# Performance work log

Measured on AMD Instinct MI355X. Metric: run time of the kernel, lower is better.

The kernel has to match this reference:

```python
import jax, jax.numpy as jnp
import numpy as np

SEQ, D_MODEL, N_HEADS, D_INT = 2048, 1024, 16, 64
D_OUT = D_MODEL // N_HEADS  # 64


def setup_inputs() -> dict:
    key = jax.random.key(0)
    ks = jax.random.split(key, 9)
    s = lambda fan_in: 1.0 / np.sqrt(fan_in)
    return {
        "input_vecs": jax.random.normal(ks[0], (8, SEQ, D_MODEL), dtype=jnp.float32),
        # weights stored [in, out] (torch Linear weight transposed)
        "Wk": jax.random.uniform(ks[1], (D_MODEL, D_INT), minval=-s(D_MODEL), maxval=s(D_MODEL)),
        "bk": jax.random.uniform(ks[2], (D_INT,), minval=-s(D_MODEL), maxval=s(D_MODEL)),
        "Wq": jax.random.uniform(ks[3], (D_MODEL, D_INT), minval=-s(D_MODEL), maxval=s(D_MODEL)),
        "bq": jax.random.uniform(ks[4], (D_INT,), minval=-s(D_MODEL), maxval=s(D_MODEL)),
        "Wv": jax.random.uniform(ks[5], (D_MODEL, D_INT), minval=-s(D_MODEL), maxval=s(D_MODEL)),
        "bv": jax.random.uniform(ks[6], (D_INT,), minval=-s(D_MODEL), maxval=s(D_MODEL)),
        "W0": jax.random.uniform(ks[7], (D_INT, D_OUT), minval=-s(D_INT), maxval=s(D_INT)),
        "b0": jax.random.uniform(ks[8], (D_OUT,), minval=-s(D_INT), maxval=s(D_INT)),
    }


def reference(input_vecs, Wk, bk, Wq, bq, Wv, bv, W0, b0):
    # Projections: [B, T, d_int]
    k = jnp.einsum("btd,de->bte", input_vecs, Wk) + bk
    q = jnp.einsum("btd,de->bte", input_vecs, Wq) + bq
    v = jnp.einsum("btd,de->bte", input_vecs, Wv) + bv
    d_k = k.shape[-1]
    # Causal scores: [B, T, T]
    scores = jnp.einsum("bqe,bke->bqk", q, k) * (d_k ** -0.5)
    T = scores.shape[-1]
    causal = jnp.tril(jnp.ones((T, T), dtype=bool))
    scores = jnp.where(causal, scores, -jnp.inf)
    attn = jax.nn.softmax(scores, axis=-1)
    ctx = jnp.einsum("bqk,bke->bqe", attn, v)  # [B, T, d_int]
    return jnp.einsum("bte,eo->bto", ctx, W0) + b0  # [B, T, d_model//num_heads]
```

## Files before the change

kernel.cpp:

```cpp
#include <hip/hip_runtime.h>
#include <math.h>

#define SEQ 2048
#define DM  1024
#define DI  64

typedef __attribute__((ext_vector_type(8))) short short8;
typedef __attribute__((ext_vector_type(4))) float f32x4;
typedef __attribute__((ext_vector_type(4))) unsigned short ush4;

#define MFMA16(a,b,c) __builtin_amdgcn_mfma_f32_16x16x32_bf16(a,b,c,0,0,0)

__device__ __forceinline__ unsigned short f2bf(float f) {
    unsigned int u = __builtin_bit_cast(unsigned int, f);
    u += 0x7fffu + ((u >> 16) & 1u);
    return (unsigned short)(u >> 16);
}


__global__ __launch_bounds__(256)
void convert_kernel(const float* __restrict__ Wq, const float* __restrict__ Wk,
                    const float* __restrict__ Wv, const float* __restrict__ W0,
                    const float* __restrict__ bq, const float* __restrict__ bk,
                    const float* __restrict__ bv,
                    unsigned short* __restrict__ Wf, unsigned short* __restrict__ W0f,
                    float* __restrict__ bcat)
{
    const int t = threadIdx.x;
    const int blk = blockIdx.x;
    if (blk < 96) {
        const int flat = blk * 256 + t;
        const int lane = flat & 63;
        const int s    = (flat >> 6) & 1;
        const int gk   = flat >> 7;
        const int g = gk >> 4, ks = gk & 15;
        const int n = lane & 15, quad = lane >> 4;
        const int ocat = 16 * g + n;
        const int mat = ocat >> 6, o = ocat & 63;
        const float* src = (mat == 0) ? Wq : (mat == 1) ? Wk : Wv;
        const float scale = (mat == 0) ? 0.125f : 1.0f;
        const int kb = ks * 64 + s * 32 + quad * 8;
        union { short8 v; unsigned short u[8]; } pk;
#pragma unroll
        for (int e = 0; e < 8; ++e)
            pk.u[e] = f2bf(src[(size_t)(kb + e) * DI + o] * scale);
        *(short8*)(Wf + (size_t)flat * 8) = pk.v;
    } else {
        const int flat = (blk - 96) * 256 + t;
        if (flat < 512) {
            const int lane = flat & 63;
            const int s    = (flat >> 6) & 1;
            const int g    = flat >> 7;
            const int n = lane & 15, quad = lane >> 4;
            const int o = 16 * g + n;
            const int kb = s * 32 + quad * 8;
            union { short8 v; unsigned short u[8]; } pk;
#pragma unroll
            for (int e = 0; e < 8; ++e)
                pk.u[e] = f2bf(W0[(size_t)(kb + e) * DI + o]);
            *(short8*)(W0f + (size_t)flat * 8) = pk.v;
        }
        if (blk == 96 && t < 192)
            bcat[t] = (t < 64) ? bq[t] * 0.125f : (t < 128) ? bk[t - 64] : bv[t - 128];
    }
}

__global__ __launch_bounds__(256, 2)
void proj_kernel(const float* __restrict__ X, const unsigned short* __restrict__ Wf,
                 const float* __restrict__ bcat,
                 unsigned short* __restrict__ Qf, unsigned short* __restrict__ Kf,
                 unsigned short* __restrict__ Vf)
{
    __shared__ alignas(16) unsigned char smem[32 * 200 * 2];
    unsigned short* XbS = (unsigned short*)smem;

    const int t = threadIdx.x;
    const int lane = t & 63, w = t >> 6;
    const int quad = lane >> 4, n = lane & 15;
    const int r0 = blockIdx.x * 32;

    const f32x4 ZERO = {0.f, 0.f, 0.f, 0.f};
    f32x4 acc[2][3];
#pragma unroll
    for (int a = 0; a < 2; ++a)
#pragma unroll
        for (int j = 0; j < 3; ++j) acc[a][j] = ZERO;

    const int srow = t >> 3, sg = t & 7;
    const int sslot = srow * 8 + (sg ^ (srow & 7));
    const float* xp = X + (size_t)(r0 + srow) * DM + sg * 8;

    for (int ks = 0; ks < 16; ++ks) {
        const int k0 = ks * 64;
        const float4 xa = *(const float4*)(xp + k0);
        const float4 xb = *(const float4*)(xp + k0 + 4);
        short8 bfr[3][2];
#pragma unroll
        for (int j = 0; j < 3; ++j)
#pragma unroll
            for (int s = 0; s < 2; ++s)
                bfr[j][s] = *(const short8*)(Wf + (size_t)((((3*w + j)*16 + ks)*2 + s)*64 + lane) * 8);
        __syncthreads();
        union { short8 v; unsigned short u[8]; } px;
        px.u[0] = f2bf(xa.x); px.u[1] = f2bf(xa.y); px.u[2] = f2bf(xa.z); px.u[3] = f2bf(xa.w);
        px.u[4] = f2bf(xb.x); px.u[5] = f2bf(xb.y); px.u[6] = f2bf(xb.z); px.u[7] = f2bf(xb.w);
        *(short8*)(XbS + sslot * 8) = px.v;
        __syncthreads();
        short8 af[2][2];
#pragma unroll
        for (int tt = 0; tt < 2; ++tt)
#pragma unroll
            for (int s = 0; s < 2; ++s) {
                const int slot = (tt*16 + n) * 8 + ((s*4 + quad) ^ (n & 7));
                af[tt][s] = *(const short8*)(XbS + slot * 8);
            }
#pragma unroll
        for (int tt = 0; tt < 2; ++tt)
#pragma unroll
            for (int j = 0; j < 3; ++j) {
                acc[tt][j] = MFMA16(af[tt][0], bfr[j][0], acc[tt][j]);
                acc[tt][j] = MFMA16(af[tt][1], bfr[j][1], acc[tt][j]);
            }
    }

    __syncthreads();
    unsigned short (*Facc)[200] = (unsigned short (*)[200])smem;
    float bias[3];
#pragma unroll
    for (int j = 0; j < 3; ++j) bias[j] = bcat[(3*w + j)*16 + n];
#pragma unroll
    for (int tt = 0; tt < 2; ++tt)
#pragma unroll
        for (int j = 0; j < 3; ++j)
#pragma unroll
            for (int r = 0; r < 4; ++r)
                Facc[tt*16 + quad*4 + r][(3*w + j)*16 + n] = f2bf(acc[tt][j][r] + bias[j]);
    __syncthreads();

    const int bidx = r0 >> 11;
    const int qt16 = (r0 >> 4) & 127;
    const int kc   = (r0 >> 6) & 31;
    const int sblk = (r0 >> 5) & 1;
    {
        const int qsel = t >> 7, s = (t >> 6) & 1, lp = t & 63;
        const int np = lp & 15, qp = lp >> 4;
        const int row = qsel * 16 + np, col = s * 32 + qp * 8;
        const size_t off = (size_t)(((bidx * 128 + qt16 + qsel) * 2 + s) * 64 + lp) * 8;
        *(short8*)(Qf + off) = *(const short8*)&Facc[row][col];
        *(short8*)(Kf + off) = *(const short8*)&Facc[row][64 + col];
    }
    {
        const int nt = t >> 6, lp = t & 63;
        const int np = lp & 15, qp = lp >> 4;
        union { short8 v; unsigned short u[8]; } ov;
#pragma unroll
        for (int e = 0; e < 8; ++e) ov.u[e] = Facc[qp * 8 + e][128 + 16 * nt + np];
        const size_t off = (size_t)((((bidx * 4 + nt) * 32 + kc) * 2 + sblk) * 64 + lp) * 8;
        *(short8*)(Vf + off) = ov.v;
    }
}

__global__ __launch_bounds__(256, 3)
void attn_kernel(const unsigned short* __restrict__ Qf, const unsigned short* __restrict__ Kf,
                 const unsigned short* __restrict__ Vf, const unsigned short* __restrict__ W0f,
                 const float* __restrict__ b0, float* __restrict__ Out)
{
    __shared__ alignas(16) float pool[4][32][72];
    __shared__ alignas(16) unsigned short Cb[32][72];
    __shared__ float Lp[4][32][4];

    const int t = threadIdx.x;
    const int lane = t & 63, w = t >> 6;
    const int quad = lane >> 4, n = lane & 15;
    const int qt = 63 - (blockIdx.x >> 3);
    const int b  = blockIdx.x & 7;
    const int q0 = qt * 32;

    unsigned short* P = (unsigned short*)&pool[w][0][0];

    short8 qf[2][2];
#pragma unroll
    for (int qh = 0; qh < 2; ++qh)
#pragma unroll
        for (int s = 0; s < 2; ++s)
            qf[qh][s] = *(const short8*)(Qf + (size_t)(((b*128 + qt*2 + qh)*2 + s)*64 + lane) * 8);

    const f32x4 ZERO = {0.f, 0.f, 0.f, 0.f};
    f32x4 ctx[2][4];
#pragma unroll
    for (int qh = 0; qh < 2; ++qh)
#pragma unroll
        for (int nt = 0; nt < 4; ++nt) ctx[qh][nt] = ZERO;
    float rs[2] = {0.f, 0.f};
    const float M0 = 8.0f;

    const int C = (qt >> 1) + 1;
    for (int kt = w; kt < C; kt += 4) {
        const int k0 = kt * 64;
        short8 kf[4][2];
#pragma unroll
        for (int tt = 0; tt < 4; ++tt)
#pragma unroll
            for (int s = 0; s < 2; ++s)
                kf[tt][s] = *(const short8*)(Kf + (size_t)(((b*128 + kt*4 + tt)*2 + s)*64 + lane) * 8);
        f32x4 sv[2][4];
#pragma unroll
        for (int qh = 0; qh < 2; ++qh)
#pragma unroll
            for (int tt = 0; tt < 4; ++tt) {
                f32x4 a = MFMA16(kf[tt][0], qf[qh][0], ZERO);
                sv[qh][tt] = MFMA16(kf[tt][1], qf[qh][1], a);
            }
        short8 vf[4][2];
#pragma unroll
        for (int nt = 0; nt < 4; ++nt)
#pragma unroll
            for (int s = 0; s < 2; ++s)
                vf[nt][s] = *(const short8*)(Vf + (size_t)((((b*4 + nt)*32 + kt)*2 + s)*64 + lane) * 8);
        if (kt == C - 1) {
#pragma unroll
            for (int qh = 0; qh < 2; ++qh)
#pragma unroll
                for (int tt = 0; tt < 4; ++tt)
#pragma unroll
                    for (int r = 0; r < 4; ++r)
                        if (k0 + 16*tt + quad*4 + r > q0 + qh*16 + n)
                            sv[qh][tt][r] = -INFINITY;
        }
#pragma unroll
        for (int qh = 0; qh < 2; ++qh)
#pragma unroll
            for (int tt = 0; tt < 4; ++tt) {
                union { ush4 v; unsigned short u[4]; } pw;
#pragma unroll
                for (int r = 0; r < 4; ++r) {
                    const float p = __expf(sv[qh][tt][r] - M0);
                    rs[qh] += p;
                    pw.u[r] = f2bf(p);
                }
                *(ush4*)&P[(size_t)(qh*16 + n) * 72 + 16*tt + quad*4] = pw.v;
            }
#pragma unroll
        for (int s = 0; s < 2; ++s) {
            const short8 pf0 = *(const short8*)&P[(size_t)(n)      * 72 + s*32 + quad*8];
            const short8 pf1 = *(const short8*)&P[(size_t)(16 + n) * 72 + s*32 + quad*8];
#pragma unroll
            for (int nt = 0; nt < 4; ++nt) {
                ctx[0][nt] = MFMA16(pf0, vf[nt][s], ctx[0][nt]);
                ctx[1][nt] = MFMA16(pf1, vf[nt][s], ctx[1][nt]);
            }
        }
    }
#pragma unroll
    for (int qh = 0; qh < 2; ++qh) {
#pragma unroll
        for (int nt = 0; nt < 4; ++nt)
#pragma unroll
            for (int r = 0; r < 4; ++r)
                pool[w][qh*16 + quad*4 + r][nt*16 + n] = ctx[qh][nt][r];
        Lp[w][qh*16 + n][quad] = rs[qh];
    }
    __syncthreads();

    {
        const int q = t >> 3, c0 = (t & 7) * 8;
        float l = 0.f;
#pragma unroll
        for (int w4 = 0; w4 < 4; ++w4)
#pragma unroll
            for (int qd = 0; qd < 4; ++qd) l += Lp[w4][q][qd];
        const float inv = 1.0f / l;
        float s[8];
#pragma unroll
        for (int j = 0; j < 8; ++j) s[j] = 0.f;
#pragma unroll
        for (int w4 = 0; w4 < 4; ++w4) {
            const float4 a = *(const float4*)&pool[w4][q][c0];
            const float4 c = *(const float4*)&pool[w4][q][c0 + 4];
            s[0] += a.x; s[1] += a.y; s[2] += a.z; s[3] += a.w;
            s[4] += c.x; s[5] += c.y; s[6] += c.z; s[7] += c.w;
        }
        union { short8 v; unsigned short u[8]; } cb;
#pragma unroll
        for (int j = 0; j < 8; ++j) cb.u[j] = f2bf(s[j] * inv);
        *(short8*)&Cb[q][c0] = cb.v;
    }
    __syncthreads();

    f32x4 oacc[2] = {ZERO, ZERO};
#pragma unroll
    for (int s = 0; s < 2; ++s) {
        const short8 wf = *(const short8*)(W0f + (size_t)((w*2 + s)*64 + lane) * 8);
#pragma unroll
        for (int tt = 0; tt < 2; ++tt) {
            const short8 cf = *(const short8*)&Cb[tt*16 + n][s*32 + quad*8];
            oacc[tt] = MFMA16(cf, wf, oacc[tt]);
        }
    }
    const float bb = b0[16*w + n];
#pragma unroll
    for (int tt = 0; tt < 2; ++tt)
#pragma unroll
        for (int r = 0; r < 4; ++r)
            Out[((size_t)b * SEQ + q0 + tt*16 + quad*4 + r) * DI + 16*w + n] = oacc[tt][r] + bb;
}

extern "C" void kernel_launch(void* const* d_in, const int* in_sizes, int n_in,
                              void* d_out, int out_size, void* d_ws, size_t ws_size,
                              hipStream_t stream) {
    const float* X  = (const float*)d_in[0];
    const float* Wk = (const float*)d_in[1];
    const float* bk = (const float*)d_in[2];
    const float* Wq = (const float*)d_in[3];
    const float* bq = (const float*)d_in[4];
    const float* Wv = (const float*)d_in[5];
    const float* bv = (const float*)d_in[6];
    const float* W0 = (const float*)d_in[7];
    const float* b0 = (const float*)d_in[8];
    float* Out = (float*)d_out;

    unsigned char* ws = (unsigned char*)d_ws;
    unsigned short* Wf   = (unsigned short*)ws;
    unsigned short* W0f  = (unsigned short*)(ws + 393216);
    float*          bcat = (float*)(ws + 401408);
    unsigned short* Qf   = (unsigned short*)(ws + 409600);
    unsigned short* Kf   = (unsigned short*)(ws + 409600 + 2097152);
    unsigned short* Vf   = (unsigned short*)(ws + 409600 + 4194304);

    convert_kernel<<<98, 256, 0, stream>>>(Wq, Wk, Wv, W0, bq, bk, bv, Wf, W0f, bcat);
    proj_kernel<<<512, 256, 0, stream>>>(X, Wf, bcat, Qf, Kf, Vf);
    attn_kernel<<<512, 256, 0, stream>>>(Qf, Kf, Vf, W0f, b0, Out);
}
```

Baseline: 134.2 us.

## Halve row tiles, double-buffer X and prefetch weights/K in proj and attention

Both the projection and attention kernels now work on 16-row tiles instead of 32 and launch twice as many blocks, with launch bounds raised to four blocks per CU. The projection kernel double-buffers the bf16 X tile in shared memory and prefetches the next weight fragments and the X rows two steps ahead, which removes one barrier per k-step. The attention kernel prefetches the next K tile in registers before computing the current one. The aim is better latency hiding and occupancy. The cost is that each MFMA fragment of K/V and weights is reused over fewer query rows, so global and L2 traffic per output rises.

```diff
diff --git a/kernel.cpp b/kernel.cpp
--- a/kernel.cpp
+++ b/kernel.cpp
@@ -65,244 +65,235 @@
     }
 }
 
-__global__ __launch_bounds__(256, 2)
+__global__ __launch_bounds__(256, 4)
 void proj_kernel(const float* __restrict__ X, const unsigned short* __restrict__ Wf,
                  const float* __restrict__ bcat,
                  unsigned short* __restrict__ Qf, unsigned short* __restrict__ Kf,
                  unsigned short* __restrict__ Vf)
 {
-    __shared__ alignas(16) unsigned char smem[32 * 200 * 2];
-    unsigned short* XbS = (unsigned short*)smem;
-
+    __shared__ alignas(16) unsigned short Xb[2][1024];
+    __shared__ alignas(16) unsigned short Facc[16][200];
     const int t = threadIdx.x;
     const int lane = t & 63, w = t >> 6;
     const int quad = lane >> 4, n = lane & 15;
-    const int r0 = blockIdx.x * 32;
+    const int r0 = blockIdx.x * 16;
+
+    const int tok = t >> 4, g = t & 15;
+    const int wslot = tok * 64 + (((g >> 1) ^ (tok & 7)) << 3) + (g & 1) * 4;
+    const float* xp = X + (size_t)(r0 + tok) * DM + g * 4;
+    const unsigned short* wbase = Wf + (size_t)(3 * w) * 16 * 1024 + lane * 8;
 
     const f32x4 ZERO = {0.f, 0.f, 0.f, 0.f};
-    f32x4 acc[2][3];
-#pragma unroll
-    for (int a = 0; a < 2; ++a)
-#pragma unroll
-        for (int j = 0; j < 3; ++j) acc[a][j] = ZERO;
-
-    const int srow = t >> 3, sg = t & 7;
-    const int sslot = srow * 8 + (sg ^ (srow & 7));
-    const float* xp = X + (size_t)(r0 + srow) * DM + sg * 8;
-
+    f32x4 acc[3] = {ZERO, ZERO, ZERO};
+
+    float4 x0 = *(const float4*)(xp);
+    float4 xA = *(const float4*)(xp + 64);
+    short8 wcur[3][2], wnxt[3][2];
+#pragma unroll
+    for (int j = 0; j < 3; ++j)
+#pragma unroll
+        for (int s = 0; s < 2; ++s)
+            wcur[j][s] = *(const short8*)(wbase + (size_t)((j * 16) * 2 + s) * 512);
+    {
+        union { ush4 v; unsigned short u[4]; } px;
+        px.u[0] = f2bf(x0.x); px.u[1] = f2bf(x0.y); px.u[2] = f2bf(x0.z); px.u[3] = f2bf(x0.w);
+        *(ush4*)&Xb[0][wslot] = px.v;
+    }
+    __syncthreads();
+
+#pragma unroll 2
     for (int ks = 0; ks < 16; ++ks) {
-        const int k0 = ks * 64;
-        const float4 xa = *(const float4*)(xp + k0);
-        const float4 xb = *(const float4*)(xp + k0 + 4);
-        short8 bfr[3][2];
+        const int kx = (ks + 2 < 16) ? ks + 2 : 15;
+        float4 xB = *(const float4*)(xp + kx * 64);
+        const int ksn = (ks + 1 < 16) ? ks + 1 : 15;
 #pragma unroll
         for (int j = 0; j < 3; ++j)
 #pragma unroll
             for (int s = 0; s < 2; ++s)
-                bfr[j][s] = *(const short8*)(Wf + (size_t)((((3*w + j)*16 + ks)*2 + s)*64 + lane) * 8);
+                wnxt[j][s] = *(const short8*)(wbase + (size_t)((j * 16 + ksn) * 2 + s) * 512);
+        short8 af[2];
+#pragma unroll
+        for (int s = 0; s < 2; ++s)
+            af[s] = *(const short8*)&Xb[ks & 1][n * 64 + (((s * 4 + quad) ^ (n & 7)) << 3)];
+#pragma unroll
+        for (int j = 0; j < 3; ++j) {
+            acc[j] = MFMA16(af[0], wcur[j][0], acc[j]);
+            acc[j] = MFMA16(af[1], wcur[j][1], acc[j]);
+        }
+        {
+            union { ush4 v; unsigned short u[4]; } px;
+            px.u[0] = f2bf(xA.x); px.u[1] = f2bf(xA.y); px.u[2] = f2bf(xA.z); px.u[3] = f2bf(xA.w);
+            *(ush4*)&Xb[(ks + 1) & 1][wslot] = px.v;
+        }
         __syncthreads();
-        union { short8 v; unsigned short u[8]; } px;
-        px.u[0] = f2bf(xa.x); px.u[1] = f2bf(xa.y); px.u[2] = f2bf(xa.z); px.u[3] = f2bf(xa.w);
-        px.u[4] = f2bf(xb.x); px.u[5] = f2bf(xb.y); px.u[6] = f2bf(xb.z); px.u[7] = f2bf(xb.w);
-        *(short8*)(XbS + sslot * 8) = px.v;
-        __syncthreads();
-        short8 af[2][2];
-#pragma unroll
-        for (int tt = 0; tt < 2; ++tt)
-#pragma unroll
-            for (int s = 0; s < 2; ++s) {
-                const int slot = (tt*16 + n) * 8 + ((s*4 + quad) ^ (n & 7));
-                af[tt][s] = *(const short8*)(XbS + slot * 8);
-            }
-#pragma unroll
-        for (int tt = 0; tt < 2; ++tt)
-#pragma unroll
-            for (int j = 0; j < 3; ++j) {
-                acc[tt][j] = MFMA16(af[tt][0], bfr[j][0], acc[tt][j]);
-                acc[tt][j] = MFMA16(af[tt][1], bfr[j][1], acc[tt][j]);
-            }
-    }
-
-    __syncthreads();
-    unsigned short (*Facc)[200] = (unsigned short (*)[200])smem;
-    float bias[3];
-#pragma unroll
-    for (int j = 0; j < 3; ++j) bias[j] = bcat[(3*w + j)*16 + n];
-#pragma unroll
-    for (int tt = 0; tt < 2; ++tt)
+        xA = xB;
 #pragma unroll
         for (int j = 0; j < 3; ++j)
 #pragma unroll
-            for (int r = 0; r < 4; ++r)
-                Facc[tt*16 + quad*4 + r][(3*w + j)*16 + n] = f2bf(acc[tt][j][r] + bias[j]);
+            for (int s = 0; s < 2; ++s) wcur[j][s] = wnxt[j][s];
+    }
+
+#pragma unroll
+    for (int j = 0; j < 3; ++j) {
+        const float bias = bcat[(3 * w + j) * 16 + n];
+#pragma unroll
+        for (int r = 0; r < 4; ++r)
+            Facc[quad * 4 + r][(3 * w + j) * 16 + n] = f2bf(acc[j][r] + bias);
+    }
     __syncthreads();
 
     const int bidx = r0 >> 11;
     const int qt16 = (r0 >> 4) & 127;
     const int kc   = (r0 >> 6) & 31;
     const int sblk = (r0 >> 5) & 1;
-    {
-        const int qsel = t >> 7, s = (t >> 6) & 1, lp = t & 63;
+    if (t < 128) {
+        const int s = t >> 6, lp = t & 63;
         const int np = lp & 15, qp = lp >> 4;
-        const int row = qsel * 16 + np, col = s * 32 + qp * 8;
-        const size_t off = (size_t)(((bidx * 128 + qt16 + qsel) * 2 + s) * 64 + lp) * 8;
-        *(short8*)(Qf + off) = *(const short8*)&Facc[row][col];
-        *(short8*)(Kf + off) = *(const short8*)&Facc[row][64 + col];
-    }
-    {
-        const int nt = t >> 6, lp = t & 63;
-        const int np = lp & 15, qp = lp >> 4;
+        const size_t off = (size_t)(((bidx * 128 + qt16) * 2 + s) * 64 + lp) * 8;
+        *(short8*)(Qf + off) = *(const short8*)&Facc[np][s * 32 + qp * 8];
+        *(short8*)(Kf + off) = *(const short8*)&Facc[np][64 + s * 32 + qp * 8];
+    } else {
+        const int i = t - 128;
+        const int nt = i >> 5, lp = i & 31;
+        const int q2 = (r0 & 31) >> 3;
+        const int quadp = q2 + (lp >> 4), np = lp & 15;
+        const int lanep = quadp * 16 + np;
         union { short8 v; unsigned short u[8]; } ov;
 #pragma unroll
-        for (int e = 0; e < 8; ++e) ov.u[e] = Facc[qp * 8 + e][128 + 16 * nt + np];
-        const size_t off = (size_t)((((bidx * 4 + nt) * 32 + kc) * 2 + sblk) * 64 + lp) * 8;
+        for (int e = 0; e < 8; ++e) ov.u[e] = Facc[(lp >> 4) * 8 + e][128 + 16 * nt + np];
+        const size_t off = (size_t)((((bidx * 4 + nt) * 32 + kc) * 2 + sblk) * 64 + lanep) * 8;
         *(short8*)(Vf + off) = ov.v;
     }
 }
 
-__global__ __launch_bounds__(256, 3)
+__global__ __launch_bounds__(256, 4)
 void attn_kernel(const unsigned short* __restrict__ Qf, const unsigned short* __restrict__ Kf,
                  const unsigned short* __restrict__ Vf, const unsigned short* __restrict__ W0f,
                  const float* __restrict__ b0, float* __restrict__ Out)
 {
-    __shared__ alignas(16) float pool[4][32][72];
-    __shared__ alignas(16) unsigned short Cb[32][72];
-    __shared__ float Lp[4][32][4];
+    __shared__ alignas(16) float pool[4][16][72];
+    __shared__ float Lp[4][16][4];
+    __shared__ alignas(16) unsigned short Cb[16][72];
 
     const int t = threadIdx.x;
     const int lane = t & 63, w = t >> 6;
     const int quad = lane >> 4, n = lane & 15;
-    const int qt = 63 - (blockIdx.x >> 3);
+    const int qt = 127 - (blockIdx.x >> 3);
     const int b  = blockIdx.x & 7;
-    const int q0 = qt * 32;
+    const int q0 = qt * 16;
 
     unsigned short* P = (unsigned short*)&pool[w][0][0];
 
-    short8 qf[2][2];
-#pragma unroll
-    for (int qh = 0; qh < 2; ++qh)
-#pragma unroll
-        for (int s = 0; s < 2; ++s)
-            qf[qh][s] = *(const short8*)(Qf + (size_t)(((b*128 + qt*2 + qh)*2 + s)*64 + lane) * 8);
+    short8 qf[2];
+#pragma unroll
+    for (int s = 0; s < 2; ++s)
+        qf[s] = *(const short8*)(Qf + (size_t)(((b * 128 + qt) * 2 + s) * 64 + lane) * 8);
 
     const f32x4 ZERO = {0.f, 0.f, 0.f, 0.f};
-    f32x4 ctx[2][4];
-#pragma unroll
-    for (int qh = 0; qh < 2; ++qh)
-#pragma unroll
-        for (int nt = 0; nt < 4; ++nt) ctx[qh][nt] = ZERO;
-    float rs[2] = {0.f, 0.f};
+    f32x4 ctx[4] = {ZERO, ZERO, ZERO, ZERO};
+    float rs = 0.f;
     const float M0 = 8.0f;
 
-    const int C = (qt >> 1) + 1;
+    const int C = (qt >> 2) + 1;
+    short8 kfc[4][2], kfn[4][2];
+    if (w < C) {
+#pragma unroll
+        for (int tt = 0; tt < 4; ++tt)
+#pragma unroll
+            for (int s = 0; s < 2; ++s)
+                kfc[tt][s] = *(const short8*)(Kf + (size_t)(((b * 128 + w * 4 + tt) * 2 + s) * 64 + lane) * 8);
+    }
     for (int kt = w; kt < C; kt += 4) {
+        const int ktn = (kt + 4 < C) ? kt + 4 : kt;
+#pragma unroll
+        for (int tt = 0; tt < 4; ++tt)
+#pragma unroll
+            for (int s = 0; s < 2; ++s)
+                kfn[tt][s] = *(const short8*)(Kf + (size_t)(((b * 128 + ktn * 4 + tt) * 2 + s) * 64 + lane) * 8);
+        short8 vf[4][2];
+#pragma unroll
+        for (int nt = 0; nt < 4; ++nt)
+#pragma unroll
+            for (int s = 0; s < 2; ++s)
+                vf[nt][s] = *(const short8*)(Vf + (size_t)((((b * 4 + nt) * 32 + kt) * 2 + s) * 64 + lane) * 8);
+
         const int k0 = kt * 64;
-        short8 kf[4][2];
+        f32x4 sv[4];
+#pragma unroll
+        for (int tt = 0; tt < 4; ++tt) {
+            f32x4 a = MFMA16(kfc[tt][0], qf[0], ZERO);
+            sv[tt] = MFMA16(kfc[tt][1], qf[1], a);
+        }
+        if (kt == C - 1) {
+#pragma unroll
+            for (int tt = 0; tt < 4; ++tt)
+#pragma unroll
+                for (int r = 0; r < 4; ++r)
+                    if (k0 + 16 * tt + quad * 4 + r > q0 + n) sv[tt][r] = -INFINITY;
+        }
+#pragma unroll
+        for (int tt = 0; tt < 4; ++tt) {
+            union { ush4 v; unsigned short u[4]; } pw;
+#pragma unroll
+            for (int r = 0; r < 4; ++r) {
+                const float p = __expf(sv[tt][r] - M0);
+                rs += p;
+                pw.u[r] = f2bf(p);
+            }
+            *(ush4*)&P[(size_t)n * 72 + 16 * tt + quad * 4] = pw.v;
+        }
+#pragma unroll
+        for (int s = 0; s < 2; ++s) {
+            const short8 pf = *(const short8*)&P[(size_t)n * 72 + s * 32 + quad * 8];
+#pragma unroll
+            for (int nt = 0; nt < 4; ++nt)
+                ctx[nt] = MFMA16(pf, vf[nt][s], ctx[nt]);
+        }
 #pragma unroll
         for (int tt = 0; tt < 4; ++tt)
 #pragma unroll
-            for (int s = 0; s < 2; ++s)
-                kf[tt][s] = *(const short8*)(Kf + (size_t)(((b*128 + kt*4 + tt)*2 + s)*64 + lane) * 8);
-        f32x4 sv[2][4];
-#pragma unroll
-        for (int qh = 0; qh < 2; ++qh)
-#pragma unroll
-            for (int tt = 0; tt < 4; ++tt) {
-                f32x4 a = MFMA16(kf[tt][0], qf[qh][0], ZERO);
-                sv[qh][tt] = MFMA16(kf[tt][1], qf[qh][1], a);
-            }
-        short8 vf[4][2];
-#pragma unroll
-        for (int nt = 0; nt < 4; ++nt)
-#pragma unroll
-            for (int s = 0; s < 2; ++s)
-                vf[nt][s] = *(const short8*)(Vf + (size_t)((((b*4 + nt)*32 + kt)*2 + s)*64 + lane) * 8);
-        if (kt == C - 1) {
-#pragma unroll
-            for (int qh = 0; qh < 2; ++qh)
-#pragma unroll
-                for (int tt = 0; tt < 4; ++tt)
-#pragma unroll
-                    for (int r = 0; r < 4; ++r)
-                        if (k0 + 16*tt + quad*4 + r > q0 + qh*16 + n)
-                            sv[qh][tt][r] = -INFINITY;
-        }
-#pragma unroll
-        for (int qh = 0; qh < 2; ++qh)
-#pragma unroll
-            for (int tt = 0; tt < 4; ++tt) {
-                union { ush4 v; unsigned short u[4]; } pw;
-#pragma unroll
-                for (int r = 0; r < 4; ++r) {
-                    const float p = __expf(sv[qh][tt][r] - M0);
-                    rs[qh] += p;
-                    pw.u[r] = f2bf(p);
-                }
-                *(ush4*)&P[(size_t)(qh*16 + n) * 72 + 16*tt + quad*4] = pw.v;
-            }
-#pragma unroll
-        for (int s = 0; s < 2; ++s) {
-            const short8 pf0 = *(const short8*)&P[(size_t)(n)      * 72 + s*32 + quad*8];
-            const short8 pf1 = *(const short8*)&P[(size_t)(16 + n) * 72 + s*32 + quad*8];
-#pragma unroll
-            for (int nt = 0; nt < 4; ++nt) {
-                ctx[0][nt] = MFMA16(pf0, vf[nt][s], ctx[0][nt]);
-                ctx[1][nt] = MFMA16(pf1, vf[nt][s], ctx[1][nt]);
-            }
-        }
-    }
-#pragma unroll
-    for (int qh = 0; qh < 2; ++qh) {
-#pragma unroll
-        for (int nt = 0; nt < 4; ++nt)
-#pragma unroll
-            for (int r = 0; r < 4; ++r)
-                pool[w][qh*16 + quad*4 + r][nt*16 + n] = ctx[qh][nt][r];
-        Lp[w][qh*16 + n][quad] = rs[qh];
-    }
+            for (int s = 0; s < 2; ++s) kfc[tt][s] = kfn[tt][s];
+    }
+#pragma unroll
+    for (int nt = 0; nt < 4; ++nt)
+#pragma unroll
+        for (int r = 0; r < 4; ++r)
+            pool[w][quad * 4 + r][nt * 16 + n] = ctx[nt][r];
+    Lp[w][n][quad] = rs;
     __syncthreads();
 
     {
-        const int q = t >> 3, c0 = (t & 7) * 8;
+        const int q = t >> 4, c0 = (t & 15) * 4;
         float l = 0.f;
 #pragma unroll
         for (int w4 = 0; w4 < 4; ++w4)
 #pragma unroll
             for (int qd = 0; qd < 4; ++qd) l += Lp[w4][q][qd];
         const float inv = 1.0f / l;
-        float s[8];
-#pragma unroll
-        for (int j = 0; j < 8; ++j) s[j] = 0.f;
+        float s[4] = {0.f, 0.f, 0.f, 0.f};
 #pragma unroll
         for (int w4 = 0; w4 < 4; ++w4) {
             const float4 a = *(const float4*)&pool[w4][q][c0];
-            const float4 c = *(const float4*)&pool[w4][q][c0 + 4];
             s[0] += a.x; s[1] += a.y; s[2] += a.z; s[3] += a.w;
-            s[4] += c.x; s[5] += c.y; s[6] += c.z; s[7] += c.w;
-        }
-        union { short8 v; unsigned short u[8]; } cb;
-#pragma unroll
-        for (int j = 0; j < 8; ++j) cb.u[j] = f2bf(s[j] * inv);
-        *(short8*)&Cb[q][c0] = cb.v;
+        }
+        union { ush4 v; unsigned short u[4]; } cb;
+#pragma unroll
+        for (int j = 0; j < 4; ++j) cb.u[j] = f2bf(s[j] * inv);
+        *(ush4*)&Cb[q][c0] = cb.v;
     }
     __syncthreads();
 
-    f32x4 oacc[2] = {ZERO, ZERO};
+    f32x4 oacc = ZERO;
 #pragma unroll
     for (int s = 0; s < 2; ++s) {
-        const short8 wf = *(const short8*)(W0f + (size_t)((w*2 + s)*64 + lane) * 8);
-#pragma unroll
-        for (int tt = 0; tt < 2; ++tt) {
-            const short8 cf = *(const short8*)&Cb[tt*16 + n][s*32 + quad*8];
-            oacc[tt] = MFMA16(cf, wf, oacc[tt]);
-        }
-    }
-    const float bb = b0[16*w + n];
-#pragma unroll
-    for (int tt = 0; tt < 2; ++tt)
-#pragma unroll
-        for (int r = 0; r < 4; ++r)
-            Out[((size_t)b * SEQ + q0 + tt*16 + quad*4 + r) * DI + 16*w + n] = oacc[tt][r] + bb;
+        const short8 cf = *(const short8*)&Cb[n][s * 32 + quad * 8];
+        const short8 wf = *(const short8*)(W0f + (size_t)((w * 2 + s) * 64 + lane) * 8);
+        oacc = MFMA16(cf, wf, oacc);
+    }
+    const float bb = b0[16 * w + n];
+#pragma unroll
+    for (int r = 0; r < 4; ++r)
+        Out[((size_t)b * SEQ + q0 + quad * 4 + r) * DI + 16 * w + n] = oacc[r] + bb;
 }
 
 extern "C" void kernel_launch(void* const* d_in, const int* in_sizes, int n_in,
@@ -328,6 +319,6 @@
     unsigned short* Vf   = (unsigned short*)(ws + 409600 + 4194304);
 
     convert_kernel<<<98, 256, 0, stream>>>(Wq, Wk, Wv, W0, bq, bk, bv, Wf, W0f, bcat);
-    proj_kernel<<<512, 256, 0, stream>>>(X, Wf, bcat, Qf, Kf, Vf);
-    attn_kernel<<<512, 256, 0, stream>>>(Qf, Kf, Vf, W0f, b0, Out);
-}
+    proj_kernel<<<1024, 256, 0, stream>>>(X, Wf, bcat, Qf, Kf, Vf);
+    attn_kernel<<<1024, 256, 0, stream>>>(Qf, Kf, Vf, W0f, b0, Out);
+}
```

Measured after the change: 144.3 us. 7.5% more time.

## Load X fragments directly into registers with software-pipelined prefetch in projection

Applied to the files above, without the earlier changes.

The projection kernel no longer stages X through shared memory with two barriers per k-step. Each wave loads its own X fragments from global memory straight into MFMA operand layout and converts them to bf16 in registers. X is prefetched two steps ahead and weights one step ahead to hide global latency. This raises register pressure, and each of the four waves now reads and converts the full X tile redundantly, which means four times the global X loads per block.

```diff
diff --git a/kernel.cpp b/kernel.cpp
--- a/kernel.cpp
+++ b/kernel.cpp
@@ -71,70 +71,99 @@
                  unsigned short* __restrict__ Qf, unsigned short* __restrict__ Kf,
                  unsigned short* __restrict__ Vf)
 {
-    __shared__ alignas(16) unsigned char smem[32 * 200 * 2];
-    unsigned short* XbS = (unsigned short*)smem;
-
+    __shared__ alignas(16) unsigned short Facc[32][200];
     const int t = threadIdx.x;
     const int lane = t & 63, w = t >> 6;
     const int quad = lane >> 4, n = lane & 15;
     const int r0 = blockIdx.x * 32;
 
+    const float* xr[2];
+    xr[0] = X + (size_t)(r0 + n) * DM + quad * 8;
+    xr[1] = X + (size_t)(r0 + 16 + n) * DM + quad * 8;
+    const unsigned short* wbase = Wf + (size_t)(3 * w) * 16 * 1024 + lane * 8;
+
     const f32x4 ZERO = {0.f, 0.f, 0.f, 0.f};
     f32x4 acc[2][3];
 #pragma unroll
-    for (int a = 0; a < 2; ++a)
-#pragma unroll
-        for (int j = 0; j < 3; ++j) acc[a][j] = ZERO;
-
-    const int srow = t >> 3, sg = t & 7;
-    const int sslot = srow * 8 + (sg ^ (srow & 7));
-    const float* xp = X + (size_t)(r0 + srow) * DM + sg * 8;
+    for (int th = 0; th < 2; ++th)
+#pragma unroll
+        for (int j = 0; j < 3; ++j) acc[th][j] = ZERO;
+
+    float4 xA[2][2][2], xB[2][2][2];
+    short8 wcur[3][2], wnxt[3][2];
+#pragma unroll
+    for (int th = 0; th < 2; ++th)
+#pragma unroll
+        for (int s = 0; s < 2; ++s) {
+            xA[th][s][0] = *(const float4*)(xr[th] + s * 32);
+            xA[th][s][1] = *(const float4*)(xr[th] + s * 32 + 4);
+            xB[th][s][0] = *(const float4*)(xr[th] + 64 + s * 32);
+            xB[th][s][1] = *(const float4*)(xr[th] + 64 + s * 32 + 4);
+        }
+#pragma unroll
+    for (int j = 0; j < 3; ++j)
+#pragma unroll
+        for (int s = 0; s < 2; ++s)
+            wcur[j][s] = *(const short8*)(wbase + (size_t)((j * 16) * 2 + s) * 512);
 
     for (int ks = 0; ks < 16; ++ks) {
-        const int k0 = ks * 64;
-        const float4 xa = *(const float4*)(xp + k0);
-        const float4 xb = *(const float4*)(xp + k0 + 4);
-        short8 bfr[3][2];
+        const int ksn = (ks + 1 < 16) ? ks + 1 : 15;
+        const int kx  = (ks + 2 < 16) ? ks + 2 : 15;
 #pragma unroll
         for (int j = 0; j < 3; ++j)
 #pragma unroll
             for (int s = 0; s < 2; ++s)
-                bfr[j][s] = *(const short8*)(Wf + (size_t)((((3*w + j)*16 + ks)*2 + s)*64 + lane) * 8);
-        __syncthreads();
-        union { short8 v; unsigned short u[8]; } px;
-        px.u[0] = f2bf(xa.x); px.u[1] = f2bf(xa.y); px.u[2] = f2bf(xa.z); px.u[3] = f2bf(xa.w);
-        px.u[4] = f2bf(xb.x); px.u[5] = f2bf(xb.y); px.u[6] = f2bf(xb.z); px.u[7] = f2bf(xb.w);
-        *(short8*)(XbS + sslot * 8) = px.v;
-        __syncthreads();
+                wnxt[j][s] = *(const short8*)(wbase + (size_t)((j * 16 + ksn) * 2 + s) * 512);
+        float4 xC[2][2][2];
+#pragma unroll
+        for (int th = 0; th < 2; ++th)
+#pragma unroll
+            for (int s = 0; s < 2; ++s) {
+                xC[th][s][0] = *(const float4*)(xr[th] + kx * 64 + s * 32);
+                xC[th][s][1] = *(const float4*)(xr[th] + kx * 64 + s * 32 + 4);
+            }
         short8 af[2][2];
 #pragma unroll
-        for (int tt = 0; tt < 2; ++tt)
+        for (int th = 0; th < 2; ++th)
 #pragma unroll
             for (int s = 0; s < 2; ++s) {
-                const int slot = (tt*16 + n) * 8 + ((s*4 + quad) ^ (n & 7));
-                af[tt][s] = *(const short8*)(XbS + slot * 8);
-            }
-#pragma unroll
-        for (int tt = 0; tt < 2; ++tt)
+                union { short8 v; unsigned short u[8]; } px;
+                px.u[0] = f2bf(xA[th][s][0].x); px.u[1] = f2bf(xA[th][s][0].y);
+                px.u[2] = f2bf(xA[th][s][0].z); px.u[3] = f2bf(xA[th][s][0].w);
+                px.u[4] = f2bf(xA[th][s][1].x); px.u[5] = f2bf(xA[th][s][1].y);
+                px.u[6] = f2bf(xA[th][s][1].z); px.u[7] = f2bf(xA[th][s][1].w);
+                af[th][s] = px.v;
+            }
+#pragma unroll
+        for (int th = 0; th < 2; ++th)
 #pragma unroll
             for (int j = 0; j < 3; ++j) {
-                acc[tt][j] = MFMA16(af[tt][0], bfr[j][0], acc[tt][j]);
-                acc[tt][j] = MFMA16(af[tt][1], bfr[j][1], acc[tt][j]);
-            }
-    }
-
-    __syncthreads();
-    unsigned short (*Facc)[200] = (unsigned short (*)[200])smem;
+                acc[th][j] = MFMA16(af[th][0], wcur[j][0], acc[th][j]);
+                acc[th][j] = MFMA16(af[th][1], wcur[j][1], acc[th][j]);
+            }
+#pragma unroll
+        for (int th = 0; th < 2; ++th)
+#pragma unroll
+            for (int s = 0; s < 2; ++s) {
+                xA[th][s][0] = xB[th][s][0]; xA[th][s][1] = xB[th][s][1];
+                xB[th][s][0] = xC[th][s][0]; xB[th][s][1] = xC[th][s][1];
+            }
+#pragma unroll
+        for (int j = 0; j < 3; ++j)
+#pragma unroll
+            for (int s = 0; s < 2; ++s) wcur[j][s] = wnxt[j][s];
+    }
+
     float bias[3];
 #pragma unroll
-    for (int j = 0; j < 3; ++j) bias[j] = bcat[(3*w + j)*16 + n];
-#pragma unroll
-    for (int tt = 0; tt < 2; ++tt)
+    for (int j = 0; j < 3; ++j) bias[j] = bcat[(3 * w + j) * 16 + n];
+#pragma unroll
+    for (int th = 0; th < 2; ++th)
 #pragma unroll
         for (int j = 0; j < 3; ++j)
 #pragma unroll
             for (int r = 0; r < 4; ++r)
-                Facc[tt*16 + quad*4 + r][(3*w + j)*16 + n] = f2bf(acc[tt][j][r] + bias[j]);
+                Facc[th * 16 + quad * 4 + r][(3 * w + j) * 16 + n] = f2bf(acc[th][j][r] + bias[j]);
     __syncthreads();
 
     const int bidx = r0 >> 11;
```

Result: slower. 228.1 us (+70.0%).

## Pre-convert X to bf16 MFMA fragment layout and simplify projection kernel

Applied to the files above, without the earlier changes.

Moves the fp32-to-bf16 conversion of the input activations out of the projection kernel into the convert pass, writing X in MFMA fragment order to a workspace buffer. The projection kernel then loads A and B fragments straight from global memory with no LDS staging or per-step barriers. It uses 16-row tiles, a 1024-block grid and higher occupancy. The cost is an extra round trip of a 32 MB bf16 X buffer through global memory (64 MB fp32 read, 32 MB written, then 32 MB read back), plus a larger convert launch.

```diff
diff --git a/kernel.cpp b/kernel.cpp
--- a/kernel.cpp
+++ b/kernel.cpp
@@ -19,12 +19,13 @@
 
 
 __global__ __launch_bounds__(256)
-void convert_kernel(const float* __restrict__ Wq, const float* __restrict__ Wk,
+void convert_kernel(const float* __restrict__ X,
+                    const float* __restrict__ Wq, const float* __restrict__ Wk,
                     const float* __restrict__ Wv, const float* __restrict__ W0,
                     const float* __restrict__ bq, const float* __restrict__ bk,
                     const float* __restrict__ bv,
                     unsigned short* __restrict__ Wf, unsigned short* __restrict__ W0f,
-                    float* __restrict__ bcat)
+                    unsigned short* __restrict__ Xf, float* __restrict__ bcat)
 {
     const int t = threadIdx.x;
     const int blk = blockIdx.x;
@@ -45,7 +46,7 @@
         for (int e = 0; e < 8; ++e)
             pk.u[e] = f2bf(src[(size_t)(kb + e) * DI + o] * scale);
         *(short8*)(Wf + (size_t)flat * 8) = pk.v;
-    } else {
+    } else if (blk < 98) {
         const int flat = (blk - 96) * 256 + t;
         if (flat < 512) {
             const int lane = flat & 63;
@@ -62,100 +63,92 @@
         }
         if (blk == 96 && t < 192)
             bcat[t] = (t < 64) ? bq[t] * 0.125f : (t < 128) ? bk[t - 64] : bv[t - 128];
-    }
-}
-
-__global__ __launch_bounds__(256, 2)
-void proj_kernel(const float* __restrict__ X, const unsigned short* __restrict__ Wf,
+    } else {
+        const int gid = (blk - 98) * 256 + t;
+        const int lane = gid & 63;
+        const int s    = (gid >> 6) & 1;
+        const int gk   = gid >> 7;
+        const int g16 = gk >> 4, ks = gk & 15;
+        const int n = lane & 15, quad = lane >> 4;
+        const int row = g16 * 16 + n;
+        const int k = ks * 64 + s * 32 + quad * 8;
+        const float4 a = *(const float4*)(X + (size_t)row * DM + k);
+        const float4 c = *(const float4*)(X + (size_t)row * DM + k + 4);
+        union { short8 v; unsigned short u[8]; } pk;
+        pk.u[0] = f2bf(a.x); pk.u[1] = f2bf(a.y); pk.u[2] = f2bf(a.z); pk.u[3] = f2bf(a.w);
+        pk.u[4] = f2bf(c.x); pk.u[5] = f2bf(c.y); pk.u[6] = f2bf(c.z); pk.u[7] = f2bf(c.w);
+        *(short8*)(Xf + (size_t)gid * 8) = pk.v;
+    }
+}
+
+__global__ __launch_bounds__(256, 4)
+void proj_kernel(const unsigned short* __restrict__ Xf, const unsigned short* __restrict__ Wf,
                  const float* __restrict__ bcat,
                  unsigned short* __restrict__ Qf, unsigned short* __restrict__ Kf,
                  unsigned short* __restrict__ Vf)
 {
-    __shared__ alignas(16) unsigned char smem[32 * 200 * 2];
-    unsigned short* XbS = (unsigned short*)smem;
-
+    __shared__ alignas(16) unsigned short Facc[16][200];
     const int t = threadIdx.x;
     const int lane = t & 63, w = t >> 6;
     const int quad = lane >> 4, n = lane & 15;
-    const int r0 = blockIdx.x * 32;
+    const int g16 = blockIdx.x;
+    const int r0 = g16 * 16;
+
+    const unsigned short* abase = Xf + (size_t)g16 * 16384 + lane * 8;
+    const unsigned short* wb0 = Wf + (size_t)(3 * w + 0) * 16384 + lane * 8;
+    const unsigned short* wb1 = Wf + (size_t)(3 * w + 1) * 16384 + lane * 8;
+    const unsigned short* wb2 = Wf + (size_t)(3 * w + 2) * 16384 + lane * 8;
 
     const f32x4 ZERO = {0.f, 0.f, 0.f, 0.f};
-    f32x4 acc[2][3];
-#pragma unroll
-    for (int a = 0; a < 2; ++a)
-#pragma unroll
-        for (int j = 0; j < 3; ++j) acc[a][j] = ZERO;
-
-    const int srow = t >> 3, sg = t & 7;
-    const int sslot = srow * 8 + (sg ^ (srow & 7));
-    const float* xp = X + (size_t)(r0 + srow) * DM + sg * 8;
-
+    f32x4 acc[3] = {ZERO, ZERO, ZERO};
+
+#pragma unroll 4
     for (int ks = 0; ks < 16; ++ks) {
-        const int k0 = ks * 64;
-        const float4 xa = *(const float4*)(xp + k0);
-        const float4 xb = *(const float4*)(xp + k0 + 4);
-        short8 bfr[3][2];
-#pragma unroll
-        for (int j = 0; j < 3; ++j)
-#pragma unroll
-            for (int s = 0; s < 2; ++s)
-                bfr[j][s] = *(const short8*)(Wf + (size_t)((((3*w + j)*16 + ks)*2 + s)*64 + lane) * 8);
-        __syncthreads();
-        union { short8 v; unsigned short u[8]; } px;
-        px.u[0] = f2bf(xa.x); px.u[1] = f2bf(xa.y); px.u[2] = f2bf(xa.z); px.u[3] = f2bf(xa.w);
-        px.u[4] = f2bf(xb.x); px.u[5] = f2bf(xb.y); px.u[6] = f2bf(xb.z); px.u[7] = f2bf(xb.w);
-        *(short8*)(XbS + sslot * 8) = px.v;
-        __syncthreads();
-        short8 af[2][2];
-#pragma unroll
-        for (int tt = 0; tt < 2; ++tt)
-#pragma unroll
-            for (int s = 0; s < 2; ++s) {
-                const int slot = (tt*16 + n) * 8 + ((s*4 + quad) ^ (n & 7));
-                af[tt][s] = *(const short8*)(XbS + slot * 8);
-            }
-#pragma unroll
-        for (int tt = 0; tt < 2; ++tt)
-#pragma unroll
-            for (int j = 0; j < 3; ++j) {
-                acc[tt][j] = MFMA16(af[tt][0], bfr[j][0], acc[tt][j]);
-                acc[tt][j] = MFMA16(af[tt][1], bfr[j][1], acc[tt][j]);
-            }
-    }
-
-    __syncthreads();
-    unsigned short (*Facc)[200] = (unsigned short (*)[200])smem;
-    float bias[3];
-#pragma unroll
-    for (int j = 0; j < 3; ++j) bias[j] = bcat[(3*w + j)*16 + n];
-#pragma unroll
-    for (int tt = 0; tt < 2; ++tt)
-#pragma unroll
-        for (int j = 0; j < 3; ++j)
-#pragma unroll
-            for (int r = 0; r < 4; ++r)
-                Facc[tt*16 + quad*4 + r][(3*w + j)*16 + n] = f2bf(acc[tt][j][r] + bias[j]);
+        short8 af[2], bf[3][2];
+#pragma unroll
+        for (int s = 0; s < 2; ++s) {
+            const size_t o = (size_t)(ks * 2 + s) * 512;
+            af[s]    = *(const short8*)(abase + o);
+            bf[0][s] = *(const short8*)(wb0 + o);
+            bf[1][s] = *(const short8*)(wb1 + o);
+            bf[2][s] = *(const short8*)(wb2 + o);
+        }
+#pragma unroll
+        for (int j = 0; j < 3; ++j) {
+            acc[j] = MFMA16(af[0], bf[j][0], acc[j]);
+            acc[j] = MFMA16(af[1], bf[j][1], acc[j]);
+        }
+    }
+
+#pragma unroll
+    for (int j = 0; j < 3; ++j) {
+        const float bias = bcat[(3 * w + j) * 16 + n];
+#pragma unroll
+        for (int r = 0; r < 4; ++r)
+            Facc[quad * 4 + r][(3 * w + j) * 16 + n] = f2bf(acc[j][r] + bias);
+    }
     __syncthreads();
 
     const int bidx = r0 >> 11;
     const int qt16 = (r0 >> 4) & 127;
     const int kc   = (r0 >> 6) & 31;
     const int sblk = (r0 >> 5) & 1;
-    {
-        const int qsel = t >> 7, s = (t >> 6) & 1, lp = t & 63;
+    if (t < 128) {
+        const int s = t >> 6, lp = t & 63;
         const int np = lp & 15, qp = lp >> 4;
-        const int row = qsel * 16 + np, col = s * 32 + qp * 8;
-        const size_t off = (size_t)(((bidx * 128 + qt16 + qsel) * 2 + s) * 64 + lp) * 8;
-        *(short8*)(Qf + off) = *(const short8*)&Facc[row][col];
-        *(short8*)(Kf + off) = *(const short8*)&Facc[row][64 + col];
-    }
-    {
-        const int nt = t >> 6, lp = t & 63;
-        const int np = lp & 15, qp = lp >> 4;
+        const size_t off = (size_t)(((bidx * 128 + qt16) * 2 + s) * 64 + lp) * 8;
+        *(short8*)(Qf + off) = *(const short8*)&Facc[np][s * 32 + qp * 8];
+        *(short8*)(Kf + off) = *(const short8*)&Facc[np][64 + s * 32 + qp * 8];
+    } else {
+        const int i = t - 128;
+        const int nt = i >> 5, lp = i & 31;
+        const int q2 = (r0 & 31) >> 3;
+        const int quadp = q2 + (lp >> 4), np = lp & 15;
+        const int lanep = quadp * 16 + np;
         union { short8 v; unsigned short u[8]; } ov;
 #pragma unroll
-        for (int e = 0; e < 8; ++e) ov.u[e] = Facc[qp * 8 + e][128 + 16 * nt + np];
-        const size_t off = (size_t)((((bidx * 4 + nt) * 32 + kc) * 2 + sblk) * 64 + lp) * 8;
+        for (int e = 0; e < 8; ++e) ov.u[e] = Facc[(lp >> 4) * 8 + e][128 + 16 * nt + np];
+        const size_t off = (size_t)((((bidx * 4 + nt) * 32 + kc) * 2 + sblk) * 64 + lanep) * 8;
         *(short8*)(Vf + off) = ov.v;
     }
 }
@@ -326,8 +319,10 @@
     unsigned short* Qf   = (unsigned short*)(ws + 409600);
     unsigned short* Kf   = (unsigned short*)(ws + 409600 + 2097152);
     unsigned short* Vf   = (unsigned short*)(ws + 409600 + 4194304);
-
-    convert_kernel<<<98, 256, 0, stream>>>(Wq, Wk, Wv, W0, bq, bk, bv, Wf, W0f, bcat);
-    proj_kernel<<<512, 256, 0, stream>>>(X, Wf, bcat, Qf, Kf, Vf);
+    unsigned short* Xf   = (unsigned short*)(ws + 8388608);
+
+    convert_kernel<<<8290, 256, 0, stream>>>(X, Wq, Wk, Wv, W0, bq, bk, bv,
+                                             Wf, W0f, Xf, bcat);
+    proj_kernel<<<1024, 256, 0, stream>>>(Xf, Wf, bcat, Qf, Kf, Vf);
     attn_kernel<<<512, 256, 0, stream>>>(Qf, Kf, Vf, W0f, b0, Out);
 }
```

New measurement: 142.2 us. 6.0% more time.
